# Optimization experiments

Measured on AMD Instinct MI355X. Metric: run time of the kernel, lower is better.

## Reference

```python
import jax, jax.numpy as jnp
import numpy as np

N_STATES = 64   # n_dice
N_OBS = 128     # number of distinct roll values (rows of log_likelihood table)
T = 262144      # sequence length


def setup_inputs() -> dict:
    key = jax.random.key(0)
    k1, k2, k3 = jax.random.split(key, 3)
    rolls = jax.random.randint(k1, (T,), 0, N_OBS)
    # torch.nn.init.normal(param, -1, 0.1): mean -1, std 0.1
    transition = jax.random.normal(k2, (N_STATES, N_STATES + 1), dtype=jnp.float32) * 0.1 - 1.0
    # emission log-likelihood table [n_obs, n_states]
    loglik_table = jax.nn.log_softmax(
        jax.random.normal(k3, (N_OBS, N_STATES), dtype=jnp.float32), axis=0)
    return {"rolls": rolls, "transition": transition, "loglik_table": loglik_table}


def reference(rolls, transition, loglik_table):
    """Viterbi decode: returns (path, final_score).

    Faithful to CRF.forward / _viterbi_algorithm, including the quirk that the
    emission vector ll_t is added along the PREVIOUS-state axis
    (roll.view(1,-1) broadcast over prev states), and that the returned path is
    in reverse-time order [s_{T-1}, ..., s_0].
    """
    S = transition.shape[0]
    ll = loglik_table[rolls]                 # [T, S]
    trans = transition[:, :S]                # [S, S]  (next, prev)
    init_delta = transition[:, S] + ll[0]    # [S]     start scores

    def step(delta, ll_t):
        # scores[next, prev] = trans[next, prev] + ll_t[prev] + delta[prev]
        scores = trans + (ll_t + delta)[None, :]
        bp = jnp.argmax(scores, axis=1)      # [S] backpointers
        return jnp.max(scores, axis=1), bp

    final_delta, bps = jax.lax.scan(step, init_delta, ll[1:])  # bps: [T-1, S]
    final_state = jnp.argmax(final_delta)
    final_score = final_delta[final_state]

    def back(state, bp_t):
        prev = bp_t[state]
        return prev, prev

    # reverse-time backtrack; ys[t] = decoded state at time t (t = 0..T-2)
    _, ys = jax.lax.scan(back, final_state, bps, reverse=True)
    path = jnp.concatenate([final_state[None], ys[::-1]])  # [s_{T-1},...,s_0]
    return path, final_score
```

## Files before the change

kernel.cpp:

```cpp
#include <hip/hip_runtime.h>
#include <hip/hip_fp16.h>
#include <stdint.h>

#define T_LEN 262144
#define S 64
#define SP1 65

#define L_FWD 32
#define W_FWD 4
#define C_FWD (T_LEN / L_FWD)
#define C_PER_XCD (C_FWD / 8)

#define LB2 8
#define VB2 8
#define NW (T_LEN / LB2)
#define PITCH (LB2 + 2)

template <int CTRL>
__device__ __forceinline__ unsigned int dpp_umin_step(unsigned int v) {
    unsigned int t = (unsigned int)__builtin_amdgcn_update_dpp(
        (int)v, (int)v, CTRL, 0xf, 0xf, false);
    return min(t, v);
}

__device__ __forceinline__ float readlane_f(float v, int lane) {
    return __int_as_float(__builtin_amdgcn_readlane(__float_as_int(v), lane));
}

__device__ __forceinline__ unsigned int pack_key(float a, int j) {
    return (__float_as_uint(a) & 0xFFFFFFC0u) | (unsigned)j;
}

__global__ __launch_bounds__(256, 8) void k1_forward(
    const int* __restrict__ rolls, const float* __restrict__ trans,
    const float* __restrict__ ll,
    unsigned int* __restrict__ bp4, int* __restrict__ wsFinal,
    float* __restrict__ out_score) {
    __shared__ __half strans_h[S * S];
    __shared__ float srowmin[S];
    __shared__ float sMc[S];
    const int tid = threadIdx.x;
    const int lane = tid & 63;
    const int wv = tid >> 6;

    if (blockIdx.x == 0 && tid == 0)
        out_score[0] = 0.0f;

    for (int k = tid; k < S * S; k += 256)
        strans_h[k] = __float2half(trans[(k & 63) * SP1 + (k >> 6)]);
    __syncthreads();

    {
        int i = tid >> 2, q = tid & 3;
        float mn = 3.0e38f;
        #pragma unroll
        for (int u = 0; u < 16; ++u)
            mn = fminf(mn, __half2float(strans_h[((q * 16 + u) << 6) | i]));
        mn = fminf(mn, __shfl_xor(mn, 1));
        mn = fminf(mn, __shfl_xor(mn, 2));
        if (q == 0) srowmin[i] = mn;
    }
    __syncthreads();
    {
        int j = tid >> 2, q = tid & 3;
        float mc = 3.0e38f;
        #pragma unroll
        for (int u = 0; u < 16; ++u) {
            int i = q * 16 + u;
            mc = fminf(mc, srowmin[i] - __half2float(strans_h[(j << 6) | i]));
        }
        mc = fminf(mc, __shfl_xor(mc, 1));
        mc = fminf(mc, __shfl_xor(mc, 2));
        if (q == 0) sMc[j] = mc;
    }
    __syncthreads();
    const float mcol = sMc[lane];

    const int c = (blockIdx.x & 7) * C_PER_XCD + (blockIdx.x >> 3) * 4 + wv;
    const int beg_out = c * L_FWD;
    int t0 = beg_out - W_FWD;
    if (t0 < 1) t0 = 1;

    int vroll = rolls[min(t0 + lane, T_LEN - 1)];

    float delta;
    if (c == 0) {
        delta = trans[lane * SP1 + S] + ll[rolls[0] * S + lane];
    } else {
        delta = 0.0f;
    }

    int r0 = __builtin_amdgcn_readlane(vroll, 0);
    int r1 = __builtin_amdgcn_readlane(vroll, 1);
    float ll_cur = ll[r0 * S + lane];
    float ll_nxt = ll[r1 * S + lane];

    int idx = 0;

    auto step = [&]() -> unsigned int {
        int rp = __builtin_amdgcn_readlane(vroll, idx + 2);
        float ll_new = ll[rp * S + lane];

        float cvec = delta + ll_cur;

        unsigned int kv = pack_key(cvec, lane);
        kv = dpp_umin_step<0x111>(kv);
        kv = dpp_umin_step<0x112>(kv);
        kv = dpp_umin_step<0x114>(kv);
        kv = dpp_umin_step<0x118>(kv);
        kv = dpp_umin_step<0x142>(kv);
        kv = dpp_umin_step<0x143>(kv);
        unsigned int kmin =
            (unsigned int)__builtin_amdgcn_readlane((int)kv, 63);

        const int jm = (int)(kmin & 63u);
        float h0 = __half2float(strans_h[(jm << 6) | lane]);
        float cjm = readlane_f(cvec, jm);
        float thr = __uint_as_float(kmin & 0xFFFFFFC0u) + mcol;
        unsigned int m = pack_key(h0 + cjm, jm);

        unsigned long long mask = __ballot(cvec >= thr) & ~(1ull << jm);
        if (mask) {
            int j1 = __ffsll(mask) - 1;
            unsigned long long rm = mask & (mask - 1);
            float a1 = __half2float(strans_h[(j1 << 6) | lane]) +
                       readlane_f(cvec, j1);
            m = min(m, pack_key(a1, j1));
            while (rm) {
                int j = __ffsll(rm) - 1;
                rm &= (rm - 1);
                float a = __half2float(strans_h[(j << 6) | lane]) +
                          readlane_f(cvec, j);
                m = min(m, pack_key(a, j));
            }
        }

        delta = __uint_as_float(m & 0xFFFFFFC0u);
        ll_cur = ll_nxt;
        ll_nxt = ll_new;
        ++idx;
        return m;
    };

    if (c != 0) {
        #pragma unroll
        for (int w = 0; w < W_FWD; ++w)
            (void)step();
    }

    const int qb = beg_out >> 2;
    unsigned int pk[8];
    {
        unsigned int p = 0u;
        int u0 = (c == 0) ? 1 : 0;
        for (int u = u0; u < 4; ++u) {
            unsigned int m = step();
            p = (p >> 8) | ((m & 63u) << 24);
        }
        pk[0] = p;
    }
    #pragma unroll
    for (int q = 1; q < 8; ++q) {
        unsigned int p = 0u;
        #pragma unroll
        for (int u = 0; u < 4; ++u) {
            unsigned int m = step();
            p = (p >> 8) | ((m & 63u) << 24);
        }
        pk[q] = p;
    }
    #pragma unroll
    for (int q = 0; q < 8; ++q)
        bp4[(unsigned)((qb + q) << 6) | (unsigned)lane] = pk[q];

    if (c == C_FWD - 1) {
        float fmx = delta;
        for (int off = 32; off; off >>= 1)
            fmx = fmaxf(fmx, __shfl_xor(fmx, off));
        unsigned long long em = __ballot(delta == fmx);
        if (lane == 0)
            *wsFinal = __ffsll(em) - 1;
    }
}

__global__ __launch_bounds__(256) void k2_backtrack(
    const unsigned int* __restrict__ bp4, const int* __restrict__ wsFinal,
    const int* __restrict__ rolls, const float* __restrict__ trans,
    const float* __restrict__ ll, float* __restrict__ out_path,
    float* __restrict__ out_score) {
    __shared__ int sst[256 * PITCH];
    __shared__ float spart[4];
    const int tid = threadIdx.x;
    const int grp = (blockIdx.x & 7) * 16 + (blockIdx.x >> 3);
    const int b = grp * 256 + tid;
    const int tlo = b * LB2;
    const int thi = tlo + LB2 - 1;
    int te = thi + VB2;
    int s;
    if (te >= T_LEN - 1) {
        te = T_LEN - 1;
        s = *wsFinal;
    } else {
        s = 0;
    }
    int* row = sst + tid * PITCH;
    #pragma unroll
    for (int u = 0; u < LB2 + VB2 - 1; ++u) {
        int t = te - u;
        if (t > tlo) {
            if (t <= thi + 1) row[t - tlo] = s;
            unsigned int w = bp4[((unsigned)(t >> 2) << 6) | (unsigned)s];
            s = (int)((w >> ((t & 3) << 3)) & 63u);
        }
    }
    row[0] = s;
    __syncthreads();

    #pragma unroll
    for (int u = 0; u < LB2; ++u)
        out_path[T_LEN - 1 - (tlo + u)] = (float)row[u];

    float acc = 0.0f;
    #pragma unroll
    for (int u = 1; u <= LB2; ++u) {
        int t = tlo + u;
        if (t <= T_LEN - 1) {
            int sp = row[u - 1];
            int st = (u == LB2)
                         ? ((tid < 255) ? sst[(tid + 1) * PITCH] : row[LB2])
                         : row[u];
            acc += trans[st * SP1 + sp] + ll[rolls[t] * S + sp];
        }
    }
    if (b == 0) {
        int s0 = row[0];
        acc += trans[s0 * SP1 + S] + ll[rolls[0] * S + s0];
    }

    for (int off = 32; off; off >>= 1)
        acc += __shfl_xor(acc, off);
    if ((tid & 63) == 0) spart[tid >> 6] = acc;
    __syncthreads();
    if (tid == 0)
        atomicAdd(out_score, (spart[0] + spart[1]) + (spart[2] + spart[3]));
}

extern "C" void kernel_launch(void* const* d_in, const int* in_sizes, int n_in,
                              void* d_out, int out_size, void* d_ws, size_t ws_size,
                              hipStream_t stream) {
    const int* rolls = (const int*)d_in[0];
    const float* trans = (const float*)d_in[1];
    const float* ll = (const float*)d_in[2];
    float* out = (float*)d_out;
    char* ws = (char*)d_ws;
    int* wsFinal = (int*)(ws + 8);
    unsigned int* bp4 = (unsigned int*)(ws + 2048);

    k1_forward<<<C_FWD / 4, 256, 0, stream>>>(rolls, trans, ll, bp4, wsFinal,
                                              out + T_LEN);
    k2_backtrack<<<NW / 256, 256, 0, stream>>>(bp4, wsFinal, rolls, trans, ll,
                                               out, out + T_LEN);
}
```

Measured before the change: 112.5 us.

## Interleave two Viterbi chunks per wave, shorten chunks, use fp32 transitions, smaller backtrack blocks

Each forward wave now processes two independent 16-step chunks in lockstep, interleaving their DPP argmax reductions and loads so the latency of one chain can hide behind the other. Chunk length drops from 32 to 16 with the same warm-up of 4, so total thread count stays the same but warm-up overhead per output step grows. The transition table in LDS moves from fp16 to fp32, which removes conversions and changes pruning precision. The backtrack kernel uses 64-thread blocks and drops the cross-wave shared reduction in exchange for more atomics.

```diff
diff --git a/kernel.cpp b/kernel.cpp
--- a/kernel.cpp
+++ b/kernel.cpp
@@ -1,12 +1,11 @@
 #include <hip/hip_runtime.h>
-#include <hip/hip_fp16.h>
 #include <stdint.h>
 
 #define T_LEN 262144
 #define S 64
 #define SP1 65
 
-#define L_FWD 32
+#define L_FWD 16
 #define W_FWD 4
 #define C_FWD (T_LEN / L_FWD)
 #define C_PER_XCD (C_FWD / 8)
@@ -14,6 +13,8 @@
 #define LB2 8
 #define VB2 8
 #define NW (T_LEN / LB2)
+#define K2_TPB 64
+#define K2_BLK (NW / K2_TPB)
 #define PITCH (LB2 + 2)
 
 template <int CTRL>
@@ -31,12 +32,17 @@
     return (__float_as_uint(a) & 0xFFFFFFC0u) | (unsigned)j;
 }
 
+struct Ch {
+    float delta, ll_cur, ll_nxt;
+    int vroll, idx;
+};
+
 __global__ __launch_bounds__(256, 8) void k1_forward(
     const int* __restrict__ rolls, const float* __restrict__ trans,
     const float* __restrict__ ll,
     unsigned int* __restrict__ bp4, int* __restrict__ wsFinal,
     float* __restrict__ out_score) {
-    __shared__ __half strans_h[S * S];
+    __shared__ float strans_f[S * S];
     __shared__ float srowmin[S];
     __shared__ float sMc[S];
     const int tid = threadIdx.x;
@@ -47,7 +53,7 @@
         out_score[0] = 0.0f;
 
     for (int k = tid; k < S * S; k += 256)
-        strans_h[k] = __float2half(trans[(k & 63) * SP1 + (k >> 6)]);
+        strans_f[k] = trans[(k & 63) * SP1 + (k >> 6)];
     __syncthreads();
 
     {
@@ -55,7 +61,7 @@
         float mn = 3.0e38f;
         #pragma unroll
         for (int u = 0; u < 16; ++u)
-            mn = fminf(mn, __half2float(strans_h[((q * 16 + u) << 6) | i]));
+            mn = fminf(mn, strans_f[((q * 16 + u) << 6) | i]);
         mn = fminf(mn, __shfl_xor(mn, 1));
         mn = fminf(mn, __shfl_xor(mn, 2));
         if (q == 0) srowmin[i] = mn;
@@ -67,7 +73,7 @@
         #pragma unroll
         for (int u = 0; u < 16; ++u) {
             int i = q * 16 + u;
-            mc = fminf(mc, srowmin[i] - __half2float(strans_h[(j << 6) | i]));
+            mc = fminf(mc, srowmin[i] - strans_f[(j << 6) | i]);
         }
         mc = fminf(mc, __shfl_xor(mc, 1));
         mc = fminf(mc, __shfl_xor(mc, 2));
@@ -76,33 +82,28 @@
     __syncthreads();
     const float mcol = sMc[lane];
 
-    const int c = (blockIdx.x & 7) * C_PER_XCD + (blockIdx.x >> 3) * 4 + wv;
-    const int beg_out = c * L_FWD;
-    int t0 = beg_out - W_FWD;
-    if (t0 < 1) t0 = 1;
-
-    int vroll = rolls[min(t0 + lane, T_LEN - 1)];
-
-    float delta;
-    if (c == 0) {
-        delta = trans[lane * SP1 + S] + ll[rolls[0] * S + lane];
-    } else {
-        delta = 0.0f;
-    }
-
-    int r0 = __builtin_amdgcn_readlane(vroll, 0);
-    int r1 = __builtin_amdgcn_readlane(vroll, 1);
-    float ll_cur = ll[r0 * S + lane];
-    float ll_nxt = ll[r1 * S + lane];
-
-    int idx = 0;
-
-    auto step = [&]() -> unsigned int {
-        int rp = __builtin_amdgcn_readlane(vroll, idx + 2);
-        float ll_new = ll[rp * S + lane];
-
-        float cvec = delta + ll_cur;
-
+    const int cA = (blockIdx.x & 7) * C_PER_XCD + (blockIdx.x >> 3) * 8 + wv * 2;
+    const int cB = cA + 1;
+
+    Ch A, B;
+    auto init = [&](Ch& C, int c) {
+        int t0 = c * L_FWD - W_FWD;
+        if (t0 < 1) t0 = 1;
+        C.vroll = rolls[min(t0 + lane, T_LEN - 1)];
+        if (c == 0)
+            C.delta = trans[lane * SP1 + S] + ll[rolls[0] * S + lane];
+        else
+            C.delta = 0.0f;
+        int r0 = __builtin_amdgcn_readlane(C.vroll, 0);
+        int r1 = __builtin_amdgcn_readlane(C.vroll, 1);
+        C.ll_cur = ll[r0 * S + lane];
+        C.ll_nxt = ll[r1 * S + lane];
+        C.idx = 0;
+    };
+    init(A, cA);
+    init(B, cB);
+
+    auto argmax_red = [&](float cvec) -> unsigned int {
         unsigned int kv = pack_key(cvec, lane);
         kv = dpp_umin_step<0x111>(kv);
         kv = dpp_umin_step<0x112>(kv);
@@ -110,89 +111,117 @@
         kv = dpp_umin_step<0x118>(kv);
         kv = dpp_umin_step<0x142>(kv);
         kv = dpp_umin_step<0x143>(kv);
-        unsigned int kmin =
-            (unsigned int)__builtin_amdgcn_readlane((int)kv, 63);
-
-        const int jm = (int)(kmin & 63u);
-        float h0 = __half2float(strans_h[(jm << 6) | lane]);
-        float cjm = readlane_f(cvec, jm);
-        float thr = __uint_as_float(kmin & 0xFFFFFFC0u) + mcol;
-        unsigned int m = pack_key(h0 + cjm, jm);
-
-        unsigned long long mask = __ballot(cvec >= thr) & ~(1ull << jm);
+        return (unsigned int)__builtin_amdgcn_readlane((int)kv, 63);
+    };
+
+    auto tail = [&](Ch& C, float cvec, unsigned long long mask,
+                    unsigned int m, float ll_new) -> unsigned int {
         if (mask) {
             int j1 = __ffsll(mask) - 1;
             unsigned long long rm = mask & (mask - 1);
-            float a1 = __half2float(strans_h[(j1 << 6) | lane]) +
-                       readlane_f(cvec, j1);
+            float a1 = strans_f[(j1 << 6) | lane] + readlane_f(cvec, j1);
             m = min(m, pack_key(a1, j1));
             while (rm) {
                 int j = __ffsll(rm) - 1;
                 rm &= (rm - 1);
-                float a = __half2float(strans_h[(j << 6) | lane]) +
-                          readlane_f(cvec, j);
+                float a = strans_f[(j << 6) | lane] + readlane_f(cvec, j);
                 m = min(m, pack_key(a, j));
             }
         }
-
-        delta = __uint_as_float(m & 0xFFFFFFC0u);
-        ll_cur = ll_nxt;
-        ll_nxt = ll_new;
-        ++idx;
+        C.delta = __uint_as_float(m & 0xFFFFFFC0u);
+        C.ll_cur = C.ll_nxt;
+        C.ll_nxt = ll_new;
+        C.idx++;
         return m;
     };
 
-    if (c != 0) {
-        #pragma unroll
+    auto pair = [&](unsigned int& mA, unsigned int& mB) {
+        float cva = A.delta + A.ll_cur;
+        float cvb = B.delta + B.ll_cur;
+        unsigned int ka = argmax_red(cva);
+        unsigned int kb = argmax_red(cvb);
+        int rpa = __builtin_amdgcn_readlane(A.vroll, A.idx + 2);
+        int rpb = __builtin_amdgcn_readlane(B.vroll, B.idx + 2);
+        float lna = ll[rpa * S + lane];
+        float lnb = ll[rpb * S + lane];
+        int jma = (int)(ka & 63u), jmb = (int)(kb & 63u);
+        float h0a = strans_f[(jma << 6) | lane];
+        float h0b = strans_f[(jmb << 6) | lane];
+        float thra = __uint_as_float(ka & 0xFFFFFFC0u) + mcol;
+        float thrb = __uint_as_float(kb & 0xFFFFFFC0u) + mcol;
+        unsigned long long ma_ = __ballot(cva >= thra) & ~(1ull << jma);
+        unsigned long long mb_ = __ballot(cvb >= thrb) & ~(1ull << jmb);
+        unsigned int pa = pack_key(h0a + readlane_f(cva, jma), jma);
+        unsigned int pb = pack_key(h0b + readlane_f(cvb, jmb), jmb);
+        mA = tail(A, cva, ma_, pa, lna);
+        mB = tail(B, cvb, mb_, pb, lnb);
+    };
+
+    auto one = [&](Ch& C) -> unsigned int {
+        float cv = C.delta + C.ll_cur;
+        unsigned int k = argmax_red(cv);
+        int rp = __builtin_amdgcn_readlane(C.vroll, C.idx + 2);
+        float ln = ll[rp * S + lane];
+        int jm = (int)(k & 63u);
+        float h0 = strans_f[(jm << 6) | lane];
+        float thr = __uint_as_float(k & 0xFFFFFFC0u) + mcol;
+        unsigned long long mk = __ballot(cv >= thr) & ~(1ull << jm);
+        unsigned int p = pack_key(h0 + readlane_f(cv, jm), jm);
+        return tail(C, cv, mk, p, ln);
+    };
+
+    const bool a0 = (cA == 0);
+
+    if (!a0) {
+        #pragma unroll 1
+        for (int w = 0; w < W_FWD; ++w) {
+            unsigned int ma, mb;
+            pair(ma, mb);
+        }
+    } else {
+        #pragma unroll 1
         for (int w = 0; w < W_FWD; ++w)
-            (void)step();
-    }
-
-    const int qb = beg_out >> 2;
-    unsigned int pk[8];
-    {
-        unsigned int p = 0u;
-        int u0 = (c == 0) ? 1 : 0;
-        for (int u = u0; u < 4; ++u) {
-            unsigned int m = step();
-            p = (p >> 8) | ((m & 63u) << 24);
-        }
-        pk[0] = p;
-    }
-    #pragma unroll
-    for (int q = 1; q < 8; ++q) {
-        unsigned int p = 0u;
-        #pragma unroll
+            (void)one(B);
+    }
+
+    #pragma unroll 1
+    for (int q = 0; q < 4; ++q) {
+        unsigned int pA = 0u, pB = 0u;
+        #pragma unroll 1
         for (int u = 0; u < 4; ++u) {
-            unsigned int m = step();
-            p = (p >> 8) | ((m & 63u) << 24);
-        }
-        pk[q] = p;
-    }
-    #pragma unroll
-    for (int q = 0; q < 8; ++q)
-        bp4[(unsigned)((qb + q) << 6) | (unsigned)lane] = pk[q];
-
-    if (c == C_FWD - 1) {
-        float fmx = delta;
+            if (a0 && q == 0 && u == 0) {
+                unsigned int mb = one(B);
+                pB = (pB >> 8) | ((mb & 63u) << 24);
+            } else {
+                unsigned int ma, mb;
+                pair(ma, mb);
+                pA = (pA >> 8) | ((ma & 63u) << 24);
+                pB = (pB >> 8) | ((mb & 63u) << 24);
+            }
+        }
+        bp4[(unsigned)((cA * 4 + q) << 6) | (unsigned)lane] = pA;
+        bp4[(unsigned)((cB * 4 + q) << 6) | (unsigned)lane] = pB;
+    }
+
+    if (cB == C_FWD - 1) {
+        float fmx = B.delta;
         for (int off = 32; off; off >>= 1)
             fmx = fmaxf(fmx, __shfl_xor(fmx, off));
-        unsigned long long em = __ballot(delta == fmx);
+        unsigned long long em = __ballot(B.delta == fmx);
         if (lane == 0)
             *wsFinal = __ffsll(em) - 1;
     }
 }
 
-__global__ __launch_bounds__(256) void k2_backtrack(
+__global__ __launch_bounds__(64) void k2_backtrack(
     const unsigned int* __restrict__ bp4, const int* __restrict__ wsFinal,
     const int* __restrict__ rolls, const float* __restrict__ trans,
     const float* __restrict__ ll, float* __restrict__ out_path,
     float* __restrict__ out_score) {
-    __shared__ int sst[256 * PITCH];
-    __shared__ float spart[4];
+    __shared__ int sst[K2_TPB * PITCH];
     const int tid = threadIdx.x;
-    const int grp = (blockIdx.x & 7) * 16 + (blockIdx.x >> 3);
-    const int b = grp * 256 + tid;
+    const int wb = (blockIdx.x & 7) * (K2_BLK / 8) + (blockIdx.x >> 3);
+    const int b = wb * K2_TPB + tid;
     const int tlo = b * LB2;
     const int thi = tlo + LB2 - 1;
     int te = thi + VB2;
@@ -227,7 +256,7 @@
         if (t <= T_LEN - 1) {
             int sp = row[u - 1];
             int st = (u == LB2)
-                         ? ((tid < 255) ? sst[(tid + 1) * PITCH] : row[LB2])
+                         ? ((tid < K2_TPB - 1) ? sst[(tid + 1) * PITCH] : row[LB2])
                          : row[u];
             acc += trans[st * SP1 + sp] + ll[rolls[t] * S + sp];
         }
@@ -239,10 +268,8 @@
 
     for (int off = 32; off; off >>= 1)
         acc += __shfl_xor(acc, off);
-    if ((tid & 63) == 0) spart[tid >> 6] = acc;
-    __syncthreads();
     if (tid == 0)
-        atomicAdd(out_score, (spart[0] + spart[1]) + (spart[2] + spart[3]));
+        atomicAdd(out_score, acc);
 }
 
 extern "C" void kernel_launch(void* const* d_in, const int* in_sizes, int n_in,
@@ -256,8 +283,8 @@
     int* wsFinal = (int*)(ws + 8);
     unsigned int* bp4 = (unsigned int*)(ws + 2048);
 
-    k1_forward<<<C_FWD / 4, 256, 0, stream>>>(rolls, trans, ll, bp4, wsFinal,
+    k1_forward<<<C_FWD / 8, 256, 0, stream>>>(rolls, trans, ll, bp4, wsFinal,
                                               out + T_LEN);
-    k2_backtrack<<<NW / 256, 256, 0, stream>>>(bp4, wsFinal, rolls, trans, ll,
-                                               out, out + T_LEN);
-}
+    k2_backtrack<<<K2_BLK, K2_TPB, 0, stream>>>(bp4, wsFinal, rolls, trans, ll,
+                                                out, out + T_LEN);
+}
```

After: 120.3 us. 1.07x slower.

## Compose per-chunk backpointer maps for hierarchical backtrack with LDS-staged chunks

Applied to the files above, without the earlier changes.

The forward kernel now also composes each chunk's 32 backpointer steps into a 64-entry skip map, built with ds_bpermute and stored as bytes. A new seed kernel walks these chunk-level maps with a short convergence window to find each chunk's entry state. The backtrack kernel then stages two chunks' backpointers per wave in LDS and has each lane trace its chunk from the seed, capturing its own timestep. This replaces the per-thread 8+8 step global-memory backtrack, at the cost of an extra launch and an extra bpermute per forward step.

```diff
diff --git a/kernel.cpp b/kernel.cpp
--- a/kernel.cpp
+++ b/kernel.cpp
@@ -11,10 +11,14 @@
 #define C_FWD (T_LEN / L_FWD)
 #define C_PER_XCD (C_FWD / 8)
 
-#define LB2 8
-#define VB2 8
-#define NW (T_LEN / LB2)
-#define PITCH (LB2 + 2)
+#define W1 4
+#define V1 4
+
+#define K2B_BLOCKS (C_FWD / 8)
+
+#define WS_BP_OFF 2048
+#define WS_SKIP_OFF (WS_BP_OFF + 16 * 1024 * 1024)
+#define WS_SEED_OFF (WS_SKIP_OFF + 512 * 1024)
 
 template <int CTRL>
 __device__ __forceinline__ unsigned int dpp_umin_step(unsigned int v) {
@@ -34,8 +38,8 @@
 __global__ __launch_bounds__(256, 8) void k1_forward(
     const int* __restrict__ rolls, const float* __restrict__ trans,
     const float* __restrict__ ll,
-    unsigned int* __restrict__ bp4, int* __restrict__ wsFinal,
-    float* __restrict__ out_score) {
+    unsigned int* __restrict__ bp4, unsigned char* __restrict__ skipT,
+    int* __restrict__ wsFinal, float* __restrict__ out_score) {
     __shared__ __half strans_h[S * S];
     __shared__ float srowmin[S];
     __shared__ float sMc[S];
@@ -150,12 +154,18 @@
 
     const int qb = beg_out >> 2;
     unsigned int pk[8];
+    int vmap = 0;
     {
         unsigned int p = 0u;
         int u0 = (c == 0) ? 1 : 0;
         for (int u = u0; u < 4; ++u) {
             unsigned int m = step();
-            p = (p >> 8) | ((m & 63u) << 24);
+            int bp = (int)(m & 63u);
+            p = (p >> 8) | ((unsigned)bp << 24);
+            if (u == u0)
+                vmap = bp;
+            else
+                vmap = __builtin_amdgcn_ds_bpermute(bp << 2, vmap);
         }
         pk[0] = p;
     }
@@ -165,13 +175,17 @@
         #pragma unroll
         for (int u = 0; u < 4; ++u) {
             unsigned int m = step();
-            p = (p >> 8) | ((m & 63u) << 24);
+            int bp = (int)(m & 63u);
+            p = (p >> 8) | ((unsigned)bp << 24);
+            vmap = __builtin_amdgcn_ds_bpermute(bp << 2, vmap);
         }
         pk[q] = p;
     }
     #pragma unroll
     for (int q = 0; q < 8; ++q)
         bp4[(unsigned)((qb + q) << 6) | (unsigned)lane] = pk[q];
+
+    skipT[(c << 6) | lane] = (unsigned char)vmap;
 
     if (c == C_FWD - 1) {
         float fmx = delta;
@@ -183,63 +197,77 @@
     }
 }
 
-__global__ __launch_bounds__(256) void k2_backtrack(
-    const unsigned int* __restrict__ bp4, const int* __restrict__ wsFinal,
+__global__ __launch_bounds__(256) void k2a_seed(
+    const unsigned char* __restrict__ skipT, const int* __restrict__ wsFinal,
+    unsigned char* __restrict__ Bseed) {
+    int w = blockIdx.x * 256 + threadIdx.x;
+    int clo = w * W1;
+    int chi = clo + W1 - 1;
+    int te = chi + V1;
+    int s;
+    if (te >= C_FWD - 1) {
+        te = C_FWD - 1;
+        s = *wsFinal;
+    } else {
+        s = 0;
+    }
+    #pragma unroll
+    for (int u = 0; u < W1 + V1; ++u) {
+        int c = te - u;
+        if (c >= clo) {
+            if (c <= chi) Bseed[c] = (unsigned char)s;
+            s = (int)skipT[(c << 6) | s];
+        }
+    }
+}
+
+__global__ __launch_bounds__(256) void k2b_backtrack(
+    const unsigned int* __restrict__ bp4, const unsigned char* __restrict__ Bseed,
     const int* __restrict__ rolls, const float* __restrict__ trans,
     const float* __restrict__ ll, float* __restrict__ out_path,
     float* __restrict__ out_score) {
-    __shared__ int sst[256 * PITCH];
+    __shared__ unsigned int sbp[4 * 1024];
     __shared__ float spart[4];
     const int tid = threadIdx.x;
-    const int grp = (blockIdx.x & 7) * 16 + (blockIdx.x >> 3);
-    const int b = grp * 256 + tid;
-    const int tlo = b * LB2;
-    const int thi = tlo + LB2 - 1;
-    int te = thi + VB2;
-    int s;
-    if (te >= T_LEN - 1) {
-        te = T_LEN - 1;
-        s = *wsFinal;
-    } else {
-        s = 0;
-    }
-    int* row = sst + tid * PITCH;
-    #pragma unroll
-    for (int u = 0; u < LB2 + VB2 - 1; ++u) {
-        int t = te - u;
-        if (t > tlo) {
-            if (t <= thi + 1) row[t - tlo] = s;
-            unsigned int w = bp4[((unsigned)(t >> 2) << 6) | (unsigned)s];
-            s = (int)((w >> ((t & 3) << 3)) & 63u);
-        }
-    }
-    row[0] = s;
-    __syncthreads();
-
-    #pragma unroll
-    for (int u = 0; u < LB2; ++u)
-        out_path[T_LEN - 1 - (tlo + u)] = (float)row[u];
-
-    float acc = 0.0f;
-    #pragma unroll
-    for (int u = 1; u <= LB2; ++u) {
-        int t = tlo + u;
-        if (t <= T_LEN - 1) {
-            int sp = row[u - 1];
-            int st = (u == LB2)
-                         ? ((tid < 255) ? sst[(tid + 1) * PITCH] : row[LB2])
-                         : row[u];
-            acc += trans[st * SP1 + sp] + ll[rolls[t] * S + sp];
-        }
-    }
-    if (b == 0) {
-        int s0 = row[0];
-        acc += trans[s0 * SP1 + S] + ll[rolls[0] * S + s0];
-    }
+    const int lane = tid & 63;
+    const int wv = tid >> 6;
+    const int g = (blockIdx.x & 7) * (K2B_BLOCKS / 8) + (blockIdx.x >> 3);
+    const int cA = g * 8 + wv * 2;
+    const int grp = lane >> 5;
+    const int k = lane & 31;
+    const int c = cA + grp;
+
+    unsigned int* wbase = sbp + (wv << 10);
+    #pragma unroll
+    for (int r = 0; r < 16; ++r)
+        wbase[(r << 6) | lane] = bp4[(unsigned)(((cA * 8 + r) << 6) | lane)];
+    __syncthreads();
+
+    int s = (int)Bseed[c];
+    int cap = 0;
+    const char* cbase = (const char*)(wbase + (grp << 9));
+    #pragma unroll
+    for (int d = 31; d >= 0; --d) {
+        cap = (d == k) ? s : cap;
+        s = (int)(unsigned char)
+                cbase[((d >> 2) << 8) + (s << 2) + (d & 3)];
+    }
+    int spv = __shfl_up(cap, 1);
+    if (k == 0) spv = s;
+
+    const int t = c * 32 + k;
+    out_path[T_LEN - 1 - t] = (float)cap;
+
+    int rt = rolls[t];
+    float acc;
+    if (t == 0)
+        acc = trans[cap * SP1 + S] + ll[rt * S + cap];
+    else
+        acc = trans[cap * SP1 + spv] + ll[rt * S + spv];
 
     for (int off = 32; off; off >>= 1)
         acc += __shfl_xor(acc, off);
-    if ((tid & 63) == 0) spart[tid >> 6] = acc;
+    if (lane == 0) spart[wv] = acc;
     __syncthreads();
     if (tid == 0)
         atomicAdd(out_score, (spart[0] + spart[1]) + (spart[2] + spart[3]));
@@ -254,10 +282,13 @@
     float* out = (float*)d_out;
     char* ws = (char*)d_ws;
     int* wsFinal = (int*)(ws + 8);
-    unsigned int* bp4 = (unsigned int*)(ws + 2048);
-
-    k1_forward<<<C_FWD / 4, 256, 0, stream>>>(rolls, trans, ll, bp4, wsFinal,
-                                              out + T_LEN);
-    k2_backtrack<<<NW / 256, 256, 0, stream>>>(bp4, wsFinal, rolls, trans, ll,
-                                               out, out + T_LEN);
-}
+    unsigned int* bp4 = (unsigned int*)(ws + WS_BP_OFF);
+    unsigned char* skipT = (unsigned char*)(ws + WS_SKIP_OFF);
+    unsigned char* Bseed = (unsigned char*)(ws + WS_SEED_OFF);
+
+    k1_forward<<<C_FWD / 4, 256, 0, stream>>>(rolls, trans, ll, bp4, skipT,
+                                              wsFinal, out + T_LEN);
+    k2a_seed<<<C_FWD / W1 / 256, 256, 0, stream>>>(skipT, wsFinal, Bseed);
+    k2b_backtrack<<<K2B_BLOCKS, 256, 0, stream>>>(bp4, Bseed, rolls, trans, ll,
+                                                  out, out + T_LEN);
+}
```

New measurement: 125.2 us. 1.11x slower.

## Backtrack per wavefront with register-held backpointer rows and readlane chasing

Applied to the files above, without the earlier changes.

The backtrack kernel now gives each wavefront a 32-step segment with a 12-step warm-up. It loads the needed packed backpointer rows coalesced into registers, one lane per state, and follows the pointer chain with readlane instead of dependent scattered global loads per thread. The path is captured into lanes so output writes and score accumulation are lane-parallel. This removes the serial global-memory latency chain and the shared-memory staging, at the cost of fewer threads doing the scalar chase and a shorter warm-up window (12 vs 8 per 8-step segment, relatively less redundancy).

```diff
diff --git a/kernel.cpp b/kernel.cpp
--- a/kernel.cpp
+++ b/kernel.cpp
@@ -11,10 +11,9 @@
 #define C_FWD (T_LEN / L_FWD)
 #define C_PER_XCD (C_FWD / 8)
 
-#define LB2 8
-#define VB2 8
-#define NW (T_LEN / LB2)
-#define PITCH (LB2 + 2)
+#define LB3 32
+#define VB3 12
+#define NW3 (T_LEN / LB3)
 
 template <int CTRL>
 __device__ __forceinline__ unsigned int dpp_umin_step(unsigned int v) {
@@ -183,19 +182,20 @@
     }
 }
 
-__global__ __launch_bounds__(256) void k2_backtrack(
+__global__ __launch_bounds__(256, 8) void k2_backtrack(
     const unsigned int* __restrict__ bp4, const int* __restrict__ wsFinal,
     const int* __restrict__ rolls, const float* __restrict__ trans,
     const float* __restrict__ ll, float* __restrict__ out_path,
     float* __restrict__ out_score) {
-    __shared__ int sst[256 * PITCH];
+    __shared__ int sstlo[4];
     __shared__ float spart[4];
     const int tid = threadIdx.x;
-    const int grp = (blockIdx.x & 7) * 16 + (blockIdx.x >> 3);
-    const int b = grp * 256 + tid;
-    const int tlo = b * LB2;
-    const int thi = tlo + LB2 - 1;
-    int te = thi + VB2;
+    const int lane = tid & 63;
+    const int wv = tid >> 6;
+    const int w = (blockIdx.x & 7) * C_PER_XCD + (blockIdx.x >> 3) * 4 + wv;
+    const int tlo = w * LB3;
+    const int q0 = tlo >> 2;
+    int te = tlo + LB3 + VB3 - 1;
     int s;
     if (te >= T_LEN - 1) {
         te = T_LEN - 1;
@@ -203,43 +203,66 @@
     } else {
         s = 0;
     }
-    int* row = sst + tid * PITCH;
-    #pragma unroll
-    for (int u = 0; u < LB2 + VB2 - 1; ++u) {
-        int t = te - u;
-        if (t > tlo) {
-            if (t <= thi + 1) row[t - tlo] = s;
-            unsigned int w = bp4[((unsigned)(t >> 2) << 6) | (unsigned)s];
-            s = (int)((w >> ((t & 3) << 3)) & 63u);
-        }
-    }
-    row[0] = s;
-    __syncthreads();
-
-    #pragma unroll
-    for (int u = 0; u < LB2; ++u)
-        out_path[T_LEN - 1 - (tlo + u)] = (float)row[u];
-
+    const int dte = te - tlo;
+
+    unsigned int R0 = bp4[(unsigned)(((q0 + 0) << 6) | lane)];
+    unsigned int R1 = bp4[(unsigned)(((q0 + 1) << 6) | lane)];
+    unsigned int R2 = bp4[(unsigned)(((q0 + 2) << 6) | lane)];
+    unsigned int R3 = bp4[(unsigned)(((q0 + 3) << 6) | lane)];
+    unsigned int R4 = bp4[(unsigned)(((q0 + 4) << 6) | lane)];
+    unsigned int R5 = bp4[(unsigned)(((q0 + 5) << 6) | lane)];
+    unsigned int R6 = bp4[(unsigned)(((q0 + 6) << 6) | lane)];
+    unsigned int R7 = bp4[(unsigned)(((q0 + 7) << 6) | lane)];
+    unsigned int R8 = bp4[(unsigned)(((q0 + 8) << 6) | lane)];
+    unsigned int R9 = bp4[(unsigned)(((q0 + 9) << 6) | lane)];
+    unsigned int RA = bp4[(unsigned)(((q0 + 10) << 6) | lane)];
+
+    int cap = 0;
+
+#define CHASE(DT, ROW)                                                   \
+    do {                                                                 \
+        if ((DT) <= dte) {                                               \
+            cap = (lane == (DT)) ? s : cap;                              \
+            int b_ = __builtin_amdgcn_readlane((int)(ROW), s);           \
+            s = (b_ >> (((DT) & 3) << 3)) & 63;                          \
+        }                                                                \
+    } while (0)
+
+    CHASE(43, RA); CHASE(42, RA); CHASE(41, RA); CHASE(40, RA);
+    CHASE(39, R9); CHASE(38, R9); CHASE(37, R9); CHASE(36, R9);
+    CHASE(35, R8); CHASE(34, R8); CHASE(33, R8); CHASE(32, R8);
+    CHASE(31, R7); CHASE(30, R7); CHASE(29, R7); CHASE(28, R7);
+    CHASE(27, R6); CHASE(26, R6); CHASE(25, R6); CHASE(24, R6);
+    CHASE(23, R5); CHASE(22, R5); CHASE(21, R5); CHASE(20, R5);
+    CHASE(19, R4); CHASE(18, R4); CHASE(17, R4); CHASE(16, R4);
+    CHASE(15, R3); CHASE(14, R3); CHASE(13, R3); CHASE(12, R3);
+    CHASE(11, R2); CHASE(10, R2); CHASE(9, R2);  CHASE(8, R2);
+    CHASE(7, R1);  CHASE(6, R1);  CHASE(5, R1);  CHASE(4, R1);
+    CHASE(3, R0);  CHASE(2, R0);  CHASE(1, R0);
+#undef CHASE
+    cap = (lane == 0) ? s : cap;
+
+    if (lane == 0) sstlo[wv] = s;
+    __syncthreads();
+    int bnd = (wv < 3) ? sstlo[wv + 1] : __builtin_amdgcn_readlane(cap, 32);
+
+    if (lane < 32)
+        out_path[T_LEN - 1 - (tlo + lane)] = (float)cap;
+
+    int stn = __shfl(cap, lane + 1);
+    if (lane == 31) stn = bnd;
     float acc = 0.0f;
-    #pragma unroll
-    for (int u = 1; u <= LB2; ++u) {
-        int t = tlo + u;
-        if (t <= T_LEN - 1) {
-            int sp = row[u - 1];
-            int st = (u == LB2)
-                         ? ((tid < 255) ? sst[(tid + 1) * PITCH] : row[LB2])
-                         : row[u];
-            acc += trans[st * SP1 + sp] + ll[rolls[t] * S + sp];
-        }
-    }
-    if (b == 0) {
-        int s0 = row[0];
-        acc += trans[s0 * SP1 + S] + ll[rolls[0] * S + s0];
+    if (lane < 32) {
+        int t = tlo + 1 + lane;
+        if (t <= T_LEN - 1)
+            acc = trans[stn * SP1 + cap] + ll[rolls[t] * S + cap];
+        if (w == 0 && lane == 0)
+            acc += trans[cap * SP1 + S] + ll[rolls[0] * S + cap];
     }
 
     for (int off = 32; off; off >>= 1)
         acc += __shfl_xor(acc, off);
-    if ((tid & 63) == 0) spart[tid >> 6] = acc;
+    if (lane == 0) spart[wv] = acc;
     __syncthreads();
     if (tid == 0)
         atomicAdd(out_score, (spart[0] + spart[1]) + (spart[2] + spart[3]));
@@ -258,6 +281,6 @@
 
     k1_forward<<<C_FWD / 4, 256, 0, stream>>>(rolls, trans, ll, bp4, wsFinal,
                                               out + T_LEN);
-    k2_backtrack<<<NW / 256, 256, 0, stream>>>(bp4, wsFinal, rolls, trans, ll,
-                                               out, out + T_LEN);
-}
+    k2_backtrack<<<NW3 / 4, 256, 0, stream>>>(bp4, wsFinal, rolls, trans, ll,
+                                              out, out + T_LEN);
+}
```

Result: slower. 132.6 us (+17.8%).
